# Optimization experiments

Hardware: AMD Instinct MI355X
Metric: run time of the kernel (lower is better)

Reference implementation:

```python
import jax, jax.numpy as jnp
import numpy as np

B, N, H, W, C = 4, 8, 512, 512, 65536
SCALING = 10.0
EPS = 1e-10
ITERS = 17  # 2**17 > C+1, so pointer doubling covers any tree depth


def setup_inputs() -> dict:
    key = jax.random.key(0)
    k = jax.random.split(key, 8)
    # per-component grey-level differences (already in scaled/quantized units)
    diff = jax.random.uniform(k[0], (B, N, C), jnp.float32, 0.0, 4.0)
    # raw 15 attributes: xmin,ymin,xmax,ymax,area,angle,pca_big,pca_small,hu1..7
    bbox = jax.random.uniform(k[1], (B, N, C, 4), jnp.float32, 0.0, 512.0)
    area = 1.0 + jax.random.uniform(k[2], (B, N, C, 1)) * 1e4
    angle = (jax.random.uniform(k[3], (B, N, C, 1)) - 0.5) * np.pi
    pca_big = 1e-3 + jax.random.uniform(k[4], (B, N, C, 1)) * 100.0
    pca_small = pca_big * jax.random.uniform(k[5], (B, N, C, 1))
    hu = jax.random.normal(k[6], (B, N, C, 7)) * 0.01
    attrs = jnp.concatenate([bbox, area, angle, pca_big, pca_small, hu], axis=-1)
    # topologically ordered parent pointers: parent[c] < c; root (c=0) -> sentinel C
    idx = jnp.arange(C, dtype=jnp.float32)
    u = jax.random.uniform(k[7], (B, N, C))
    parent = jnp.floor(u * idx).astype(jnp.int32)
    parent = parent.at[..., 0].set(C)
    pix2cc = jax.random.randint(jax.random.fold_in(key, 1), (B, N, H, W), 0, C, dtype=jnp.int32)
    weight = jax.random.uniform(jax.random.fold_in(key, 2), (N, 17, 1), jnp.float32, -0.01, 0.01)
    bias = jnp.zeros((N, 1), jnp.float32)
    return dict(diff=diff, attrs=attrs, weight=weight, bias=bias, parent=parent, pix2cc=pix2cc)


def _log_scaling(f):
    # faithful port of maxtree _log_scaling: 15 raw attrs -> 17 features
    lshape = jnp.sqrt(f[..., 7:8]) / (jnp.sqrt(f[..., 6:7]) + EPS)
    cosa = jnp.cos(f[..., 5:6])
    sina = jnp.sin(f[..., 5:6])
    area = jnp.log(f[..., 4:5])
    tail = jnp.log(jnp.abs(f[..., 6:]) + EPS) * jnp.sign(f[..., 6:])
    return jnp.concatenate([f[..., :4], area, tail, lshape, cosa, sina], axis=-1)


def reference(diff, attrs, weight, bias, parent, pix2cc):
    feats = _log_scaling(attrs)                                   # (B,N,C,17)
    logits = jnp.einsum('bnck,nko->bnco', feats, weight)[..., 0]  # (B,N,C)
    logits = logits + bias[None, :, :]                            # bias (N,1) broadcasts over C
    scores = jax.nn.sigmoid(logits)                               # per-component keep score
    w = diff * scores                                             # weighted level increment
    # append zero-weight self-loop sentinel so path sums terminate at the root
    wz = jnp.concatenate([w, jnp.zeros((B, N, 1), w.dtype)], axis=-1)
    pz = jnp.concatenate([parent, jnp.full((B, N, 1), C, jnp.int32)], axis=-1)
    s, ptr = wz, pz
    for _ in range(ITERS):  # pointer doubling: s[c] = sum of diff*score along root path
        s = s + jnp.take_along_axis(s, ptr, axis=-1)
        ptr = jnp.take_along_axis(ptr, ptr, axis=-1)
    val = s[..., :C]                                              # (B,N,C) reconstructed levels
    flat = jnp.take_along_axis(val, pix2cc.reshape(B, N, H * W), axis=-1)
    return flat.reshape(B, N, H, W) / SCALING
```

## Files before the change

### kernel.cpp

```cpp
#include <hip/hip_runtime.h>

#define BB 4
#define NN 8
#define HH 512
#define WW 512
#define CC 65536
#define EPSF 1e-10f
#define NF 15
#define NFE 17
#define MLOW 4096
#define PSENT 0xFFFFu

typedef unsigned int PN;

typedef int   nint4   __attribute__((ext_vector_type(4)));
typedef float nfloat4 __attribute__((ext_vector_type(4)));

__device__ inline unsigned short f2bf(float f) {
    union { float f; unsigned u; } t; t.f = f;
    unsigned u = t.u;
    return (unsigned short)((u + 0x7fffu + ((u >> 16) & 1u)) >> 16);
}
__device__ inline float bf2f(unsigned short h) {
    union { unsigned u; float f; } t; t.u = ((unsigned)h) << 16;
    return t.f;
}
__device__ inline float pn_w(PN v) { return bf2f((unsigned short)(v >> 16)); }
__device__ inline unsigned pn_p(PN v) { return v & 0xFFFFu; }

__global__ __launch_bounds__(256) void k_score(
    const float* __restrict__ diff, const float* __restrict__ attrs,
    const float* __restrict__ weight, const float* __restrict__ bias,
    const int* __restrict__ parent, PN* __restrict__ wp)
{
    __shared__ float sat[256 * NF];
    const int tid = threadIdx.x;
    const long long base = (long long)blockIdx.x * 256;
    const int n = (int)((base / CC) % NN);

    const nfloat4* src = (const nfloat4*)(attrs + base * NF);
    nfloat4* dst4 = (nfloat4*)sat;
    #pragma unroll
    for (int i = 0; i < 4; ++i) {
        int k = tid + i * 256;
        if (k < (256 * NF) / 4) dst4[k] = __builtin_nontemporal_load(src + k);
    }
    __syncthreads();

    float f[NF];
    #pragma unroll
    for (int j = 0; j < NF; ++j) f[j] = sat[tid * NF + j];

    float wgt[NFE];
    #pragma unroll
    for (int k = 0; k < NFE; ++k) wgt[k] = weight[n * NFE + k];

    float logit = bias[n];
    logit = fmaf(f[0], wgt[0], logit);
    logit = fmaf(f[1], wgt[1], logit);
    logit = fmaf(f[2], wgt[2], logit);
    logit = fmaf(f[3], wgt[3], logit);
    logit = fmaf(__logf(f[4]), wgt[4], logit);
    #pragma unroll
    for (int j = 0; j < 9; ++j) {
        float x = f[6 + j];
        float lg = __logf(fabsf(x) + EPSF);
        float t = (x > 0.f) ? lg : ((x < 0.f) ? -lg : 0.f);
        logit = fmaf(t, wgt[5 + j], logit);
    }
    logit = fmaf(sqrtf(f[7]) * __frcp_rn(sqrtf(f[6]) + EPSF), wgt[14], logit);
    logit = fmaf(__cosf(f[5]), wgt[15], logit);
    logit = fmaf(__sinf(f[5]), wgt[16], logit);

    const float score = __frcp_rn(1.f + __expf(-logit));
    const long long idx = base + tid;
    const float w = diff[idx] * score;
    const int p = parent[idx];
    const unsigned p16 = (p >= CC) ? PSENT : (unsigned)p;
    wp[idx] = ((unsigned)f2bf(w) << 16) | p16;
}

__global__ __launch_bounds__(256) void k_low(
    const PN* __restrict__ wp, float* __restrict__ valLow)
{
    const int i = blockIdx.x * 256 + threadIdx.x;
    const int tree = i >> 12;
    const int node = i & (MLOW - 1);
    const long long tbase = (long long)tree << 16;
    PN cur = wp[tbase + node];
    float acc = pn_w(cur);
    unsigned p = pn_p(cur);
    while (p != PSENT) {
        PN nx = wp[tbase + p];
        acc += pn_w(nx);
        p = pn_p(nx);
    }
    valLow[i] = acc;
}

__global__ __launch_bounds__(256) void k_chain(
    const PN* __restrict__ wp, const float* __restrict__ valLow,
    unsigned short* __restrict__ valh)
{
    const int bid = blockIdx.x;
    const int tree  = ((bid & 7) << 2) + ((bid >> 3) >> 8);
    const int chunk = (bid >> 3) & 255;
    const int node0 = (chunk << 8) + threadIdx.x;
    const long long tbase = (long long)tree << 16;
    const float* vlow = valLow + ((long long)tree << 12);

    float acc;
    if (node0 < MLOW) {
        acc = vlow[node0];
    } else {
        PN cur = wp[tbase + node0];
        acc = pn_w(cur);
        unsigned p = pn_p(cur);
        while (p >= MLOW) {
            PN nx = wp[tbase + p];
            acc += pn_w(nx);
            p = pn_p(nx);
        }
        acc += vlow[p];
    }
    valh[tbase + node0] = f2bf(acc);
}

__global__ __launch_bounds__(512) void k_gather(
    const unsigned short* __restrict__ valh, const int* __restrict__ pix,
    float* __restrict__ out)
{
    __shared__ unsigned short sval[CC];
    const int bid  = blockIdx.x;
    const int tree = bid >> 3;
    const int seg  = bid & 7;

    const uint4* s4 = (const uint4*)(valh + ((long long)tree << 16));
    uint4* d4 = (uint4*)sval;
    #pragma unroll
    for (int i = 0; i < 16; ++i)
        d4[threadIdx.x + i * 512] = s4[threadIdx.x + i * 512];
    __syncthreads();

    const long long pbase = ((long long)tree << 18) + ((long long)seg << 15);
    const nint4*   psrc = (const nint4*)(pix + pbase);
    nfloat4*       pdst = (nfloat4*)(out + pbase);
    #pragma unroll 4
    for (int it = 0; it < 16; ++it) {
        const int i4 = threadIdx.x + it * 512;
        nint4 cc = __builtin_nontemporal_load(psrc + i4);
        nfloat4 o;
        o.x = bf2f(sval[cc.x]) * 0.1f;
        o.y = bf2f(sval[cc.y]) * 0.1f;
        o.z = bf2f(sval[cc.z]) * 0.1f;
        o.w = bf2f(sval[cc.w]) * 0.1f;
        __builtin_nontemporal_store(o, pdst + i4);
    }
}

extern "C" void kernel_launch(void* const* d_in, const int* in_sizes, int n_in,
                              void* d_out, int out_size, void* d_ws, size_t ws_size,
                              hipStream_t stream) {
    const float* diff   = (const float*)d_in[0];
    const float* attrs  = (const float*)d_in[1];
    const float* weight = (const float*)d_in[2];
    const float* bias   = (const float*)d_in[3];
    const int*   parent = (const int*)d_in[4];
    const int*   pix    = (const int*)d_in[5];
    float* out = (float*)d_out;

    PN*             wp     = (PN*)d_ws;
    unsigned short* valh   = (unsigned short*)((char*)d_ws + (size_t)BB * NN * CC * sizeof(PN));
    float*          valLow = (float*)((char*)valh + (size_t)BB * NN * CC * sizeof(unsigned short));

    const long long total = (long long)BB * NN * CC;

    k_score <<<(int)(total / 256), 256, 0, stream>>>(diff, attrs, weight, bias, parent, wp);
    k_low   <<<(BB * NN * MLOW) / 256, 256, 0, stream>>>(wp, valLow);
    k_chain <<<(int)(total / 256), 256, 0, stream>>>(wp, valLow, valh);
    k_gather<<<BB * NN * 8, 512, 0, stream>>>(valh, pix, out);
}
```

Baseline: 249.4 us.

## Fuse all four stages into one cooperative kernel with grid syncs

Merges the score, low-node chain, full chain and gather kernels into a single cooperative kernel of 256 blocks of 1024 threads, separated by grid.sync barriers. The score stage now double-buffers attribute staging through LDS while computing the previous chunk. The aim is to remove three kernel launch gaps and tail effects. In exchange, parallelism drops to 256 blocks, and the low-node stage uses only 512 threads per block, so latency-bound chain walks may run with less occupancy than before.

```diff
diff --git a/kernel.cpp b/kernel.cpp
--- a/kernel.cpp
+++ b/kernel.cpp
@@ -1,4 +1,7 @@
 #include <hip/hip_runtime.h>
+#include <hip/hip_cooperative_groups.h>
+
+namespace cg = cooperative_groups;
 
 #define BB 4
 #define NN 8
@@ -11,6 +14,10 @@
 #define MLOW 4096
 #define PSENT 0xFFFFu
 
+#define THREADS 1024
+#define SCHUNKS 8
+#define STG4 (THREADS * NF / 4)
+
 typedef unsigned int PN;
 
 typedef int   nint4   __attribute__((ext_vector_type(4)));
@@ -28,133 +35,166 @@
 __device__ inline float pn_w(PN v) { return bf2f((unsigned short)(v >> 16)); }
 __device__ inline unsigned pn_p(PN v) { return v & 0xFFFFu; }
 
-__global__ __launch_bounds__(256) void k_score(
+__global__ __launch_bounds__(THREADS) void k_fused(
     const float* __restrict__ diff, const float* __restrict__ attrs,
     const float* __restrict__ weight, const float* __restrict__ bias,
-    const int* __restrict__ parent, PN* __restrict__ wp)
+    const int* __restrict__ parent, const int* __restrict__ pix,
+    float* __restrict__ out,
+    PN* __restrict__ wp, float* __restrict__ valLow,
+    unsigned short* __restrict__ valh)
 {
-    __shared__ float sat[256 * NF];
-    const int tid = threadIdx.x;
-    const long long base = (long long)blockIdx.x * 256;
-    const int n = (int)((base / CC) % NN);
-
-    const nfloat4* src = (const nfloat4*)(attrs + base * NF);
-    nfloat4* dst4 = (nfloat4*)sat;
-    #pragma unroll
-    for (int i = 0; i < 4; ++i) {
-        int k = tid + i * 256;
-        if (k < (256 * NF) / 4) dst4[k] = __builtin_nontemporal_load(src + k);
-    }
-    __syncthreads();
-
-    float f[NF];
-    #pragma unroll
-    for (int j = 0; j < NF; ++j) f[j] = sat[tid * NF + j];
-
+    __shared__ __align__(16) unsigned short sval[CC];
+
+    const int tid  = threadIdx.x;
+    const int bid  = blockIdx.x;
+    const int x    = bid & 7;
+    const int j    = bid >> 3;
+    const int tree = x * 4 + (j & 3);
+    const int g    = j >> 2;
+    const int n    = tree & 7;
+    const long long tbase = (long long)tree << 16;
+
+    cg::grid_group grid = cg::this_grid();
+
+    float* sat = (float*)sval;
     float wgt[NFE];
     #pragma unroll
     for (int k = 0; k < NFE; ++k) wgt[k] = weight[n * NFE + k];
-
-    float logit = bias[n];
-    logit = fmaf(f[0], wgt[0], logit);
-    logit = fmaf(f[1], wgt[1], logit);
-    logit = fmaf(f[2], wgt[2], logit);
-    logit = fmaf(f[3], wgt[3], logit);
-    logit = fmaf(__logf(f[4]), wgt[4], logit);
-    #pragma unroll
-    for (int j = 0; j < 9; ++j) {
-        float x = f[6 + j];
-        float lg = __logf(fabsf(x) + EPSF);
-        float t = (x > 0.f) ? lg : ((x < 0.f) ? -lg : 0.f);
-        logit = fmaf(t, wgt[5 + j], logit);
-    }
-    logit = fmaf(sqrtf(f[7]) * __frcp_rn(sqrtf(f[6]) + EPSF), wgt[14], logit);
-    logit = fmaf(__cosf(f[5]), wgt[15], logit);
-    logit = fmaf(__sinf(f[5]), wgt[16], logit);
-
-    const float score = __frcp_rn(1.f + __expf(-logit));
-    const long long idx = base + tid;
-    const float w = diff[idx] * score;
-    const int p = parent[idx];
-    const unsigned p16 = (p >= CC) ? PSENT : (unsigned)p;
-    wp[idx] = ((unsigned)f2bf(w) << 16) | p16;
-}
-
-__global__ __launch_bounds__(256) void k_low(
-    const PN* __restrict__ wp, float* __restrict__ valLow)
-{
-    const int i = blockIdx.x * 256 + threadIdx.x;
-    const int tree = i >> 12;
-    const int node = i & (MLOW - 1);
-    const long long tbase = (long long)tree << 16;
-    PN cur = wp[tbase + node];
-    float acc = pn_w(cur);
-    unsigned p = pn_p(cur);
-    while (p != PSENT) {
-        PN nx = wp[tbase + p];
-        acc += pn_w(nx);
-        p = pn_p(nx);
-    }
-    valLow[i] = acc;
-}
-
-__global__ __launch_bounds__(256) void k_chain(
-    const PN* __restrict__ wp, const float* __restrict__ valLow,
-    unsigned short* __restrict__ valh)
-{
-    const int bid = blockIdx.x;
-    const int tree  = ((bid & 7) << 2) + ((bid >> 3) >> 8);
-    const int chunk = (bid >> 3) & 255;
-    const int node0 = (chunk << 8) + threadIdx.x;
-    const long long tbase = (long long)tree << 16;
-    const float* vlow = valLow + ((long long)tree << 12);
-
-    float acc;
-    if (node0 < MLOW) {
-        acc = vlow[node0];
-    } else {
-        PN cur = wp[tbase + node0];
-        acc = pn_w(cur);
+    const float bia = bias[n];
+
+    nfloat4 r[4];
+    {
+        const nfloat4* src = (const nfloat4*)(attrs + (tbase + (long long)g * 8192) * NF);
+        #pragma unroll
+        for (int i = 0; i < 4; ++i) {
+            int k = tid + i * THREADS;
+            if (k < STG4) r[i] = __builtin_nontemporal_load(src + k);
+        }
+        nfloat4* dst = (nfloat4*)sat;
+        #pragma unroll
+        for (int i = 0; i < 4; ++i) {
+            int k = tid + i * THREADS;
+            if (k < STG4) dst[k] = r[i];
+        }
+    }
+
+    for (int c = 0; c < SCHUNKS; ++c) {
+        __syncthreads();
+
+        if (c + 1 < SCHUNKS) {
+            const nfloat4* src = (const nfloat4*)(attrs +
+                (tbase + (long long)g * 8192 + (long long)(c + 1) * THREADS) * NF);
+            #pragma unroll
+            for (int i = 0; i < 4; ++i) {
+                int k = tid + i * THREADS;
+                if (k < STG4) r[i] = __builtin_nontemporal_load(src + k);
+            }
+        }
+
+        const float* sf = sat + (c & 1) * (THREADS * NF);
+        float f[NF];
+        #pragma unroll
+        for (int q = 0; q < NF; ++q) f[q] = sf[tid * NF + q];
+
+        float logit = bia;
+        logit = fmaf(f[0], wgt[0], logit);
+        logit = fmaf(f[1], wgt[1], logit);
+        logit = fmaf(f[2], wgt[2], logit);
+        logit = fmaf(f[3], wgt[3], logit);
+        logit = fmaf(__logf(f[4]), wgt[4], logit);
+        #pragma unroll
+        for (int q = 0; q < 9; ++q) {
+            float xv = f[6 + q];
+            float lg = __logf(fabsf(xv) + EPSF);
+            float t = (xv > 0.f) ? lg : ((xv < 0.f) ? -lg : 0.f);
+            logit = fmaf(t, wgt[5 + q], logit);
+        }
+        logit = fmaf(sqrtf(f[7]) * __frcp_rn(sqrtf(f[6]) + EPSF), wgt[14], logit);
+        logit = fmaf(__cosf(f[5]), wgt[15], logit);
+        logit = fmaf(__sinf(f[5]), wgt[16], logit);
+
+        const float score = __frcp_rn(1.f + __expf(-logit));
+        const long long node = (long long)g * 8192 + (long long)c * THREADS + tid;
+        const long long idx  = tbase + node;
+        const float w = __builtin_nontemporal_load(diff + idx) * score;
+        const int   p = __builtin_nontemporal_load(parent + idx);
+        const unsigned p16 = (p >= CC) ? PSENT : (unsigned)p;
+        wp[idx] = ((unsigned)f2bf(w) << 16) | p16;
+
+        if (c + 1 < SCHUNKS) {
+            nfloat4* dst = (nfloat4*)(sat + ((c + 1) & 1) * (THREADS * NF));
+            #pragma unroll
+            for (int i = 0; i < 4; ++i) {
+                int k = tid + i * THREADS;
+                if (k < STG4) dst[k] = r[i];
+            }
+        }
+    }
+
+    __threadfence();
+    grid.sync();
+
+    if (tid < 512) {
+        const int node = g * 512 + tid;
+        PN cur = wp[tbase + node];
+        float acc = pn_w(cur);
         unsigned p = pn_p(cur);
-        while (p >= MLOW) {
+        while (p != PSENT) {
             PN nx = wp[tbase + p];
             acc += pn_w(nx);
             p = pn_p(nx);
         }
-        acc += vlow[p];
-    }
-    valh[tbase + node0] = f2bf(acc);
-}
-
-__global__ __launch_bounds__(512) void k_gather(
-    const unsigned short* __restrict__ valh, const int* __restrict__ pix,
-    float* __restrict__ out)
-{
-    __shared__ unsigned short sval[CC];
-    const int bid  = blockIdx.x;
-    const int tree = bid >> 3;
-    const int seg  = bid & 7;
-
-    const uint4* s4 = (const uint4*)(valh + ((long long)tree << 16));
-    uint4* d4 = (uint4*)sval;
-    #pragma unroll
-    for (int i = 0; i < 16; ++i)
-        d4[threadIdx.x + i * 512] = s4[threadIdx.x + i * 512];
-    __syncthreads();
-
-    const long long pbase = ((long long)tree << 18) + ((long long)seg << 15);
-    const nint4*   psrc = (const nint4*)(pix + pbase);
-    nfloat4*       pdst = (nfloat4*)(out + pbase);
-    #pragma unroll 4
-    for (int it = 0; it < 16; ++it) {
-        const int i4 = threadIdx.x + it * 512;
-        nint4 cc = __builtin_nontemporal_load(psrc + i4);
-        nfloat4 o;
-        o.x = bf2f(sval[cc.x]) * 0.1f;
-        o.y = bf2f(sval[cc.y]) * 0.1f;
-        o.z = bf2f(sval[cc.z]) * 0.1f;
-        o.w = bf2f(sval[cc.w]) * 0.1f;
-        __builtin_nontemporal_store(o, pdst + i4);
+        valLow[((long long)tree << 12) + node] = acc;
+    }
+
+    __threadfence();
+    grid.sync();
+
+    const float* vlow = valLow + ((long long)tree << 12);
+    for (int it = 0; it < SCHUNKS; ++it) {
+        const int node0 = g * 8192 + it * THREADS + tid;
+        float acc;
+        if (node0 < MLOW) {
+            acc = vlow[node0];
+        } else {
+            PN cur = wp[tbase + node0];
+            acc = pn_w(cur);
+            unsigned p = pn_p(cur);
+            while (p >= MLOW) {
+                PN nx = wp[tbase + p];
+                acc += pn_w(nx);
+                p = pn_p(nx);
+            }
+            acc += vlow[p];
+        }
+        valh[tbase + node0] = f2bf(acc);
+    }
+
+    __threadfence();
+    grid.sync();
+
+    {
+        const uint4* s4 = (const uint4*)(valh + tbase);
+        uint4* d4 = (uint4*)sval;
+        #pragma unroll
+        for (int i = 0; i < 8; ++i)
+            d4[tid + i * THREADS] = s4[tid + i * THREADS];
+        __syncthreads();
+
+        const long long pbase = ((long long)tree << 18) + ((long long)g << 15);
+        const nint4*   psrc = (const nint4*)(pix + pbase);
+        nfloat4*       pdst = (nfloat4*)(out + pbase);
+        #pragma unroll 4
+        for (int it = 0; it < 8; ++it) {
+            const int i4 = tid + it * THREADS;
+            nint4 cc = __builtin_nontemporal_load(psrc + i4);
+            nfloat4 o;
+            o.x = bf2f(sval[cc.x]) * 0.1f;
+            o.y = bf2f(sval[cc.y]) * 0.1f;
+            o.z = bf2f(sval[cc.z]) * 0.1f;
+            o.w = bf2f(sval[cc.w]) * 0.1f;
+            __builtin_nontemporal_store(o, pdst + i4);
+        }
     }
 }
 
@@ -173,10 +213,8 @@
     unsigned short* valh   = (unsigned short*)((char*)d_ws + (size_t)BB * NN * CC * sizeof(PN));
     float*          valLow = (float*)((char*)valh + (size_t)BB * NN * CC * sizeof(unsigned short));
 
-    const long long total = (long long)BB * NN * CC;
-
-    k_score <<<(int)(total / 256), 256, 0, stream>>>(diff, attrs, weight, bias, parent, wp);
-    k_low   <<<(BB * NN * MLOW) / 256, 256, 0, stream>>>(wp, valLow);
-    k_chain <<<(int)(total / 256), 256, 0, stream>>>(wp, valLow, valh);
-    k_gather<<<BB * NN * 8, 512, 0, stream>>>(valh, pix, out);
-}
+    void* args[] = { (void*)&diff, (void*)&attrs, (void*)&weight, (void*)&bias,
+                     (void*)&parent, (void*)&pix, (void*)&out,
+                     (void*)&wp, (void*)&valLow, (void*)&valh };
+    hipLaunchCooperativeKernel((void*)k_fused, dim3(256), dim3(THREADS), args, 0, stream);
+}
```

After: 580.0 us. 133% more time.

## Batch four chain walks per thread, raise low-prefix size, widen gather blocks

Applied to the files above, without the earlier changes.

k_chain now has each thread walk four node chains at once, interleaving their dependent loads to hide pointer-chasing latency, and its grid shrinks by four. The precomputed low-node prefix grows from 4096 to 8192 nodes, so chains stop earlier in exchange for more k_low work. k_gather moves to 1024-thread blocks with a tree/segment mapping that spreads trees across XCDs, and each thread handles fewer iterations. Divergence rises because one wave keeps looping until the longest of its four chains finishes.

```diff
diff --git a/kernel.cpp b/kernel.cpp
--- a/kernel.cpp
+++ b/kernel.cpp
@@ -8,7 +8,7 @@
 #define EPSF 1e-10f
 #define NF 15
 #define NFE 17
-#define MLOW 4096
+#define MLOW 8192
 #define PSENT 0xFFFFu
 
 typedef unsigned int PN;
@@ -84,7 +84,7 @@
     const PN* __restrict__ wp, float* __restrict__ valLow)
 {
     const int i = blockIdx.x * 256 + threadIdx.x;
-    const int tree = i >> 12;
+    const int tree = i >> 13;
     const int node = i & (MLOW - 1);
     const long long tbase = (long long)tree << 16;
     PN cur = wp[tbase + node];
@@ -102,52 +102,72 @@
     const PN* __restrict__ wp, const float* __restrict__ valLow,
     unsigned short* __restrict__ valh)
 {
-    const int bid = blockIdx.x;
-    const int tree  = ((bid & 7) << 2) + ((bid >> 3) >> 8);
-    const int chunk = (bid >> 3) & 255;
-    const int node0 = (chunk << 8) + threadIdx.x;
+    const int bid  = blockIdx.x;
+    const int x    = bid & 7;
+    const int j    = bid >> 3;
+    const int tree = (x << 2) + (j & 3);
+    const int grp  = j >> 2;
     const long long tbase = (long long)tree << 16;
-    const float* vlow = valLow + ((long long)tree << 12);
-
-    float acc;
-    if (node0 < MLOW) {
-        acc = vlow[node0];
-    } else {
-        PN cur = wp[tbase + node0];
-        acc = pn_w(cur);
-        unsigned p = pn_p(cur);
-        while (p >= MLOW) {
-            PN nx = wp[tbase + p];
-            acc += pn_w(nx);
-            p = pn_p(nx);
+    const float* vlow = valLow + ((long long)tree << 13);
+    const int n0 = (grp << 10) + threadIdx.x;
+
+    if ((grp << 10) < MLOW) {
+        #pragma unroll
+        for (int s = 0; s < 4; ++s) {
+            const int nd = n0 + s * 256;
+            valh[tbase + nd] = f2bf(vlow[nd]);
         }
-        acc += vlow[p];
-    }
-    valh[tbase + node0] = f2bf(acc);
-}
-
-__global__ __launch_bounds__(512) void k_gather(
+        return;
+    }
+
+    float    a0, a1, a2, a3;
+    unsigned p0, p1, p2, p3;
+    {
+        PN c0 = wp[tbase + n0];
+        PN c1 = wp[tbase + n0 + 256];
+        PN c2 = wp[tbase + n0 + 512];
+        PN c3 = wp[tbase + n0 + 768];
+        a0 = pn_w(c0); p0 = pn_p(c0);
+        a1 = pn_w(c1); p1 = pn_p(c1);
+        a2 = pn_w(c2); p2 = pn_p(c2);
+        a3 = pn_w(c3); p3 = pn_p(c3);
+    }
+    while ((p0 >= MLOW) | (p1 >= MLOW) | (p2 >= MLOW) | (p3 >= MLOW)) {
+        if (p0 >= MLOW) { PN nx = wp[tbase + p0]; a0 += pn_w(nx); p0 = pn_p(nx); }
+        if (p1 >= MLOW) { PN nx = wp[tbase + p1]; a1 += pn_w(nx); p1 = pn_p(nx); }
+        if (p2 >= MLOW) { PN nx = wp[tbase + p2]; a2 += pn_w(nx); p2 = pn_p(nx); }
+        if (p3 >= MLOW) { PN nx = wp[tbase + p3]; a3 += pn_w(nx); p3 = pn_p(nx); }
+    }
+    valh[tbase + n0      ] = f2bf(a0 + vlow[p0]);
+    valh[tbase + n0 + 256] = f2bf(a1 + vlow[p1]);
+    valh[tbase + n0 + 512] = f2bf(a2 + vlow[p2]);
+    valh[tbase + n0 + 768] = f2bf(a3 + vlow[p3]);
+}
+
+__global__ __launch_bounds__(1024) void k_gather(
     const unsigned short* __restrict__ valh, const int* __restrict__ pix,
     float* __restrict__ out)
 {
     __shared__ unsigned short sval[CC];
     const int bid  = blockIdx.x;
-    const int tree = bid >> 3;
-    const int seg  = bid & 7;
+    const int x    = bid & 7;
+    const int r    = bid >> 3;
+    const int tree = (x << 2) + (r & 3);
+    const int seg  = r >> 2;
 
     const uint4* s4 = (const uint4*)(valh + ((long long)tree << 16));
     uint4* d4 = (uint4*)sval;
     #pragma unroll
-    for (int i = 0; i < 16; ++i)
-        d4[threadIdx.x + i * 512] = s4[threadIdx.x + i * 512];
+    for (int i = 0; i < 8; ++i)
+        d4[threadIdx.x + i * 1024] = s4[threadIdx.x + i * 1024];
     __syncthreads();
 
     const long long pbase = ((long long)tree << 18) + ((long long)seg << 15);
     const nint4*   psrc = (const nint4*)(pix + pbase);
     nfloat4*       pdst = (nfloat4*)(out + pbase);
     #pragma unroll 4
-    for (int it = 0; it < 16; ++it) {
-        const int i4 = threadIdx.x + it * 512;
+    for (int it = 0; it < 8; ++it) {
+        const int i4 = threadIdx.x + it * 1024;
         nint4 cc = __builtin_nontemporal_load(psrc + i4);
         nfloat4 o;
         o.x = bf2f(sval[cc.x]) * 0.1f;
@@ -177,6 +197,6 @@
 
     k_score <<<(int)(total / 256), 256, 0, stream>>>(diff, attrs, weight, bias, parent, wp);
     k_low   <<<(BB * NN * MLOW) / 256, 256, 0, stream>>>(wp, valLow);
-    k_chain <<<(int)(total / 256), 256, 0, stream>>>(wp, valLow, valh);
-    k_gather<<<BB * NN * 8, 512, 0, stream>>>(valh, pix, out);
-}
+    k_chain <<<(int)(total / 1024), 256, 0, stream>>>(wp, valLow, valh);
+    k_gather<<<BB * NN * 8, 1024, 0, stream>>>(valh, pix, out);
+}
```

Measured after the change: 244.2 us. 2.1% less time.
